# Performance work log

Measured on AMD Instinct MI355X. Metric: run time of the kernel, lower is better.

Reference implementation:

```python
import jax, jax.numpy as jnp
import numpy as np

DIM = 768
HEADS = 12
HEAD_DIM = DIM // HEADS
SCALE = HEAD_DIM ** -0.5


def setup_inputs() -> dict:
    key = jax.random.key(0)
    ks = jax.random.split(key, 6)
    B, N, C = 2, 2048, DIM
    x = jax.random.normal(ks[0], (B, N, C), dtype=jnp.float32)
    s = C ** -0.5
    Wq = jax.random.normal(ks[1], (C, C), dtype=jnp.float32) * s
    Wk = jax.random.normal(ks[2], (C, C), dtype=jnp.float32) * s
    Wv = jax.random.normal(ks[3], (C, C), dtype=jnp.float32) * s
    Wp = jax.random.normal(ks[4], (C, C), dtype=jnp.float32) * s
    bp = jax.random.normal(ks[5], (C,), dtype=jnp.float32) * 0.01
    return {"x": x, "Wq": Wq, "Wk": Wk, "Wv": Wv, "Wp": Wp, "bp": bp}


def reference(x, Wq, Wk, Wv, Wp, bp):
    B, N, C = x.shape
    h, d = HEADS, HEAD_DIM
    # projections (no bias), split heads: (B, h, N, d)
    Q = (x @ Wq.T).reshape(B, N, h, d).transpose(0, 2, 1, 3)
    K = (x @ Wk.T).reshape(B, N, h, d).transpose(0, 2, 1, 3)
    V = (x @ Wv.T).reshape(B, N, h, d).transpose(0, 2, 1, 3)
    # averaged key: (B, h, 1, d) -> scores (B, h, N)
    K_avg = K.mean(axis=2)  # (B, h, d)
    z = jnp.einsum('bhnd,bhd->bhn', Q, K_avg) * SCALE
    attn = jax.nn.softmax(z, axis=-1)  # (B, h, N)
    # circulant gather: roll[b,h,i,j] = attn[b,h,(j-i)%N] / N
    idx = (jnp.arange(N)[None, :] - jnp.arange(N)[:, None]) % N  # (N, N)
    roll = attn[:, :, idx] / N  # (B, h, N, N)
    out = jnp.einsum('bhij,bhjd->bhid', roll, V)  # (B, h, N, d)
    out = out.transpose(0, 2, 1, 3).reshape(B, N, C)
    return out @ Wp.T + bp
```

## Files before the change

### kernel.cpp

```cpp
#include <hip/hip_runtime.h>


typedef __bf16 bf16x8 __attribute__((ext_vector_type(8)));
typedef float  f32x4  __attribute__((ext_vector_type(4)));

#define AS_GLOBAL(p) ((const __attribute__((address_space(1))) unsigned int*)(p))
#define AS_LDS(p)    ((__attribute__((address_space(3))) unsigned int*)(p))

__device__ __forceinline__ void async16(const void* g, void* l) {
    __builtin_amdgcn_global_load_lds(AS_GLOBAL(g), AS_LDS(l), 16, 0, 0);
}

struct bf4 { __bf16 a, b, c, d; };

template <int BM, int BN, int MODE>
__device__ void gemm_phase(char* smem, const __bf16* __restrict__ A,
                           const __bf16* __restrict__ Bt, void* __restrict__ Cout,
                           const float* __restrict__ bias,
                           int K, int ldA, int ldBt, int ldC, int mBase, int nBase)
{
    constexpr int BK = 64;
    constexpr int STRIDE = (BM + BN) * BK * 2;
    constexpr int WM = BM / 2, WN = BN / 2;
    constexpr int MI = WM / 16, NI = WN / 16;
    const int tid = threadIdx.x;
    const int lane = tid & 63, wid = tid >> 6;
    const int lane15 = lane & 15, quad = lane >> 4;
    const int wm = (wid & 1) * WM, wn = (wid >> 1) * WN;

    auto stage = [&](int kb, int buf) {
        __bf16* As = (__bf16*)(smem + buf * STRIDE);
        __bf16* Bs = As + BM * BK;
#pragma unroll
        for (int c0 = 0; c0 < BM * 8; c0 += 256) {
            int c = c0 + tid, row = c >> 3, slot = c & 7;
            int k8 = slot ^ (row & 7);
            async16(A + (size_t)(mBase + row) * ldA + kb + k8 * 8, As + c * 8);
        }
#pragma unroll
        for (int c0 = 0; c0 < BN * 8; c0 += 256) {
            int c = c0 + tid, row = c >> 3, slot = c & 7;
            int k8 = slot ^ (row & 7);
            async16(Bt + (size_t)(nBase + row) * ldBt + kb + k8 * 8, Bs + c * 8);
        }
    };

    f32x4 acc[MI][NI] = {};
    const int nk = K >> 6;

    stage(0, 0);
    for (int ki = 0; ki < nk; ++ki) {
        __syncthreads();
        if (ki + 1 < nk) stage((ki + 1) << 6, (ki + 1) & 1);

        __bf16* As = (__bf16*)(smem + (ki & 1) * STRIDE);
        __bf16* Bs = As + BM * BK;
#pragma unroll
        for (int ks = 0; ks < 2; ++ks) {
            bf16x8 af[MI], bv[NI];
#pragma unroll
            for (int mi = 0; mi < MI; ++mi) {
                int row = wm + mi * 16 + lane15;
                af[mi] = *(const bf16x8*)&As[row * 64 + ((ks * 4 + quad) ^ (row & 7)) * 8];
            }
#pragma unroll
            for (int ni = 0; ni < NI; ++ni) {
                int row = wn + ni * 16 + lane15;
                bv[ni] = *(const bf16x8*)&Bs[row * 64 + ((ks * 4 + quad) ^ (row & 7)) * 8];
            }
#pragma unroll
            for (int mi = 0; mi < MI; ++mi)
#pragma unroll
                for (int ni = 0; ni < NI; ++ni)
                    acc[mi][ni] = __builtin_amdgcn_mfma_f32_16x16x32_bf16(
                        af[mi], bv[ni], acc[mi][ni], 0, 0, 0);
        }
    }

#pragma unroll
    for (int mi = 0; mi < MI; ++mi)
#pragma unroll
        for (int ni = 0; ni < NI; ++ni)
#pragma unroll
            for (int r = 0; r < 4; ++r) {
                int row = mBase + wm + mi * 16 + quad * 4 + r;
                int col = nBase + wn + ni * 16 + lane15;
                float v = acc[mi][ni][r];
                if (MODE == 0) {
                    ((__bf16*)Cout)[(size_t)row * ldC + col] = (__bf16)v;
                } else if (MODE == 1) {
                    ((float*)Cout)[(size_t)row * ldC + col] = v + bias[col];
                } else {
                    int b = row >> 11;
                    if ((unsigned)(col - b * 12) < 12u)
                        ((float*)Cout)[(size_t)col * 2048 + (row & 2047)] = v;
                }
            }
}

__global__ __launch_bounds__(256)
void k_prep(const float* __restrict__ x, const float* __restrict__ Wv,
            const float* __restrict__ Wp,
            __bf16* __restrict__ xb, __bf16* __restrict__ Wvb,
            __bf16* __restrict__ Wpb, float* __restrict__ x_avg)
{
    const int bid = blockIdx.x, tid = threadIdx.x;
    __shared__ float sums[768];
    for (int c = tid; c < 768; c += 256) sums[c] = 0.f;
    __syncthreads();

    const float4* xs = (const float4*)x + (size_t)bid * 1536;
    bf4* xd = (bf4*)xb + (size_t)bid * 1536;
#pragma unroll
    for (int r = 0; r < 6; ++r) {
        int j = tid + r * 256;
        float4 v = xs[j];
        xd[j] = bf4{(__bf16)v.x, (__bf16)v.y, (__bf16)v.z, (__bf16)v.w};
        int col = (j % 192) * 4;
        atomicAdd(&sums[col + 0], v.x);
        atomicAdd(&sums[col + 1], v.y);
        atomicAdd(&sums[col + 2], v.z);
        atomicAdd(&sums[col + 3], v.w);
    }
    const float4* wv4 = (const float4*)Wv;  bf4* wvb4 = (bf4*)Wvb;
    const float4* wp4 = (const float4*)Wp;  bf4* wpb4 = (bf4*)Wpb;
    for (int t = tid; t < 288; t += 256) {
        int g = bid * 288 + t;
        float4 v = wv4[g];
        wvb4[g] = bf4{(__bf16)v.x, (__bf16)v.y, (__bf16)v.z, (__bf16)v.w};
        float4 w2 = wp4[g];
        wpb4[g] = bf4{(__bf16)w2.x, (__bf16)w2.y, (__bf16)w2.z, (__bf16)w2.w};
    }
    __syncthreads();
    const int b = bid >> 8;
    for (int c = tid; c < 768; c += 256)
        atomicAdd(&x_avg[b * 768 + c], sums[c]);
}

__global__ __launch_bounds__(256)
void k_ub(const float* __restrict__ x_avg, const float* __restrict__ Wk,
          const float* __restrict__ Wq, __bf16* __restrict__ Ub)
{
    const int bid = blockIdx.x, tid = threadIdx.x;
    const int lane = tid & 63, wid = tid >> 6;
    __shared__ float sx[768];
    __shared__ float sk[64];
    int b = bid / 12, h = bid % 12;
    for (int c = tid; c < 768; c += 256) sx[c] = x_avg[b * 768 + c];
    __syncthreads();
    for (int round = 0; round < 16; ++round) {
        int o = round * 4 + wid;
        const float* wk = Wk + (size_t)(h * 64 + o) * 768;
        float s = 0.f;
#pragma unroll
        for (int cc0 = 0; cc0 < 768; cc0 += 64) s += sx[cc0 + lane] * wk[cc0 + lane];
#pragma unroll
        for (int off = 32; off; off >>= 1) s += __shfl_down(s, off);
        if (lane == 0) sk[o] = s * (0.125f / 2048.f);
    }
    __syncthreads();
    for (int c = tid; c < 768; c += 256) {
        float s = 0.f;
#pragma unroll 16
        for (int d2 = 0; d2 < 64; ++d2)
            s += sk[d2] * Wq[(size_t)(h * 64 + d2) * 768 + c];
        Ub[(size_t)bid * 768 + c] = (__bf16)s;
    }
}

__global__ __launch_bounds__(256, 2)
void k_gemms(const __bf16* __restrict__ xb, const __bf16* __restrict__ Wvb,
             const __bf16* __restrict__ Ub, __bf16* __restrict__ VT,
             float* __restrict__ z_t)
{
    __shared__ __attribute__((aligned(16))) char smem[65536];
    const int bid = blockIdx.x;
    if (bid < 192) {
        gemm_phase<128, 128, 0>(smem, Wvb, xb, VT, nullptr, 768, 768, 768, 4096,
                                (bid / 32) * 128, (bid % 32) * 128);
    } else {
        gemm_phase<128, 64, 2>(smem, xb, Ub, z_t, nullptr, 768, 768, 768, 0,
                               (bid - 192) * 128, 0);
    }
}

__global__ __launch_bounds__(256, 2)
void k_conv(const float* __restrict__ z_t, const __bf16* __restrict__ VT,
            __bf16* __restrict__ outp)
{
    __shared__ __attribute__((aligned(16))) char smem[69760];
    __bf16 (*rep)[2056] = (__bf16(*)[2056])smem;
    float* red = (float*)(smem + 32896);
    __bf16* attn_s = (__bf16*)(smem + 65664);

    const int bid = blockIdx.x, tid = threadIdx.x;
    const int lane = tid & 63, wid = tid >> 6;
    const int lane15 = lane & 15, quad = lane >> 4;
    const int bh = bid >> 4, b = bh / 12, h = bh % 12;
    const int m0 = (bid & 15) * 128 + (wid & 1) * 64;
    const int wn = (wid >> 1) * 32;

    {
        const float* z = z_t + (size_t)bh * 2048;
        float v[8];
        float m = -1e30f;
#pragma unroll
        for (int j = 0; j < 8; ++j) { v[j] = z[tid + j * 256]; m = fmaxf(m, v[j]); }
#pragma unroll
        for (int off = 32; off; off >>= 1) m = fmaxf(m, __shfl_xor(m, off));
        if (lane == 0) red[wid] = m;
        __syncthreads();
        m = fmaxf(fmaxf(red[0], red[1]), fmaxf(red[2], red[3]));
        __syncthreads();
        float s = 0.f;
#pragma unroll
        for (int j = 0; j < 8; ++j) { v[j] = __expf(v[j] - m); s += v[j]; }
#pragma unroll
        for (int off = 32; off; off >>= 1) s += __shfl_xor(s, off);
        if (lane == 0) red[wid] = s;
        __syncthreads();
        s = red[0] + red[1] + red[2] + red[3];
        float inv = 1.f / (s * 2048.f);
#pragma unroll
        for (int j = 0; j < 8; ++j)
            attn_s[tid + j * 256] = (__bf16)(v[j] * inv);
    }
    __syncthreads();
    for (int idx = tid; idx < 8 * 2048; idx += 256) {
        int a = idx >> 11, u = idx & 2047;
        rep[a][u] = attn_s[(u + a) & 2047];
    }

    const __bf16* vsrc = VT + (size_t)h * 64 * 4096 + b * 2048;

    auto stage = [&](int kb, int buf) {
        __bf16* vt = (__bf16*)(smem + 32896 + buf * 16384);
#pragma unroll
        for (int c0 = 0; c0 < 1024; c0 += 256) {
            int c = c0 + tid, dd = c >> 4, slot = c & 15;
            int k8 = slot ^ (dd & 15);
            async16(vsrc + (size_t)dd * 4096 + kb * 128 + k8 * 8, vt + c * 8);
        }
    };

    f32x4 acc[4][2] = {};
    stage(0, 0);
    for (int kb = 0; kb < 16; ++kb) {
        __syncthreads();
        if (kb + 1 < 16) stage(kb + 1, (kb + 1) & 1);
        __bf16* vt = (__bf16*)(smem + 32896 + (kb & 1) * 16384);

#pragma unroll
        for (int ks = 0; ks < 4; ++ks) {
            int kloc = ks * 32 + quad * 8;
            int kglob = kb * 128 + kloc;
            bf16x8 af[4], bv[2];
#pragma unroll
            for (int mi = 0; mi < 4; ++mi) {
                int m = m0 + mi * 16 + lane15;
                int p = (kglob - m) & 2047;
                int al = p & 7;
                af[mi] = *(const bf16x8*)&rep[al][p - al];
            }
#pragma unroll
            for (int ni = 0; ni < 2; ++ni) {
                int dd = wn + ni * 16 + lane15;
                int slot = (ks * 4 + quad) ^ (dd & 15);
                bv[ni] = *(const bf16x8*)&vt[dd * 128 + slot * 8];
            }
#pragma unroll
            for (int mi = 0; mi < 4; ++mi)
#pragma unroll
                for (int ni = 0; ni < 2; ++ni)
                    acc[mi][ni] = __builtin_amdgcn_mfma_f32_16x16x32_bf16(
                        af[mi], bv[ni], acc[mi][ni], 0, 0, 0);
        }
    }

#pragma unroll
    for (int mi = 0; mi < 4; ++mi)
#pragma unroll
        for (int ni = 0; ni < 2; ++ni)
#pragma unroll
            for (int r = 0; r < 4; ++r) {
                int i = m0 + mi * 16 + quad * 4 + r;
                int dd = wn + ni * 16 + lane15;
                outp[(size_t)(b * 2048 + i) * 768 + h * 64 + dd] =
                    (__bf16)acc[mi][ni][r];
            }
}

__global__ __launch_bounds__(256, 2)
void k_out(const __bf16* __restrict__ out_pre, const __bf16* __restrict__ Wpb,
           const float* __restrict__ bp, float* __restrict__ out)
{
    __shared__ __attribute__((aligned(16))) char smem[65536];
    const int bid = blockIdx.x;
    gemm_phase<128, 128, 1>(smem, out_pre, Wpb, out, bp, 768, 768, 768, 768,
                            (bid / 6) * 128, (bid % 6) * 128);
}

extern "C" void kernel_launch(void* const* d_in, const int* in_sizes, int n_in,
                              void* d_out, int out_size, void* d_ws, size_t ws_size,
                              hipStream_t stream)
{
    (void)in_sizes; (void)n_in; (void)out_size; (void)ws_size;
    const float* x  = (const float*)d_in[0];
    const float* Wq = (const float*)d_in[1];
    const float* Wk = (const float*)d_in[2];
    const float* Wv = (const float*)d_in[3];
    const float* Wp = (const float*)d_in[4];
    const float* bp = (const float*)d_in[5];

    char* w = (char*)d_ws;
    auto alloc = [&](size_t bytes) {
        char* p = w; w += (bytes + 255) & ~(size_t)255; return p;
    };
    float*  x_avg   = (float*) alloc((size_t)2 * 768 * 4);
    __bf16* xb      = (__bf16*)alloc((size_t)4096 * 768 * 2);
    __bf16* Wvb     = (__bf16*)alloc((size_t)768 * 768 * 2);
    __bf16* Wpb     = (__bf16*)alloc((size_t)768 * 768 * 2);
    __bf16* Ub      = (__bf16*)alloc((size_t)64 * 768 * 2);
    float*  z_t     = (float*) alloc((size_t)24 * 2048 * 4);
    __bf16* VT      = (__bf16*)alloc((size_t)768 * 4096 * 2);
    __bf16* out_pre = (__bf16*)alloc((size_t)4096 * 768 * 2);

    hipMemsetAsync(x_avg, 0, 2 * 768 * sizeof(float), stream);
    k_prep <<<512, 256, 0, stream>>>(x, Wv, Wp, xb, Wvb, Wpb, x_avg);
    k_ub   <<<24,  256, 0, stream>>>(x_avg, Wk, Wq, Ub);
    k_gemms<<<224, 256, 0, stream>>>(xb, Wvb, Ub, VT, z_t);
    k_conv <<<384, 256, 0, stream>>>(z_t, VT, out_pre);
    k_out  <<<192, 256, 0, stream>>>(out_pre, Wpb, bp, (float*)d_out);
}
```

Before: 159.7 us.

## Fuse key-average projection into mid kernel and drop atomics and memset

The column-sum of x is now done with deterministic per-block partial sums written to a workspace, replacing the shared and global atomics and the memset. The separate k_ub kernel is folded into the mid kernel: 96 extra blocks each recompute the averaged key and the U vector for one (b,h), then compute z for 512 tokens with a direct dot product, where before an MFMA GEMM with mostly wasted columns was used. This removes two launches and the wasted GEMM work, but each of the 4 blocks per head redundantly recomputes U from fp32 Wk and Wq, and 64 blocks of k_prep take on an extra serial 64-row reduction.

```diff
diff --git a/kernel.cpp b/kernel.cpp
--- a/kernel.cpp
+++ b/kernel.cpp
@@ -88,12 +88,8 @@
                 float v = acc[mi][ni][r];
                 if (MODE == 0) {
                     ((__bf16*)Cout)[(size_t)row * ldC + col] = (__bf16)v;
-                } else if (MODE == 1) {
+                } else {
                     ((float*)Cout)[(size_t)row * ldC + col] = v + bias[col];
-                } else {
-                    int b = row >> 11;
-                    if ((unsigned)(col - b * 12) < 12u)
-                        ((float*)Cout)[(size_t)col * 2048 + (row & 2047)] = v;
                 }
             }
 }
@@ -102,12 +98,9 @@
 void k_prep(const float* __restrict__ x, const float* __restrict__ Wv,
             const float* __restrict__ Wp,
             __bf16* __restrict__ xb, __bf16* __restrict__ Wvb,
-            __bf16* __restrict__ Wpb, float* __restrict__ x_avg)
+            __bf16* __restrict__ Wpb, float* __restrict__ x_part)
 {
     const int bid = blockIdx.x, tid = threadIdx.x;
-    __shared__ float sums[768];
-    for (int c = tid; c < 768; c += 256) sums[c] = 0.f;
-    __syncthreads();
 
     const float4* xs = (const float4*)x + (size_t)bid * 1536;
     bf4* xd = (bf4*)xb + (size_t)bid * 1536;
@@ -116,11 +109,6 @@
         int j = tid + r * 256;
         float4 v = xs[j];
         xd[j] = bf4{(__bf16)v.x, (__bf16)v.y, (__bf16)v.z, (__bf16)v.w};
-        int col = (j % 192) * 4;
-        atomicAdd(&sums[col + 0], v.x);
-        atomicAdd(&sums[col + 1], v.y);
-        atomicAdd(&sums[col + 2], v.z);
-        atomicAdd(&sums[col + 3], v.w);
     }
     const float4* wv4 = (const float4*)Wv;  bf4* wvb4 = (bf4*)Wvb;
     const float4* wp4 = (const float4*)Wp;  bf4* wpb4 = (bf4*)Wpb;
@@ -131,57 +119,88 @@
         float4 w2 = wp4[g];
         wpb4[g] = bf4{(__bf16)w2.x, (__bf16)w2.y, (__bf16)w2.z, (__bf16)w2.w};
     }
-    __syncthreads();
-    const int b = bid >> 8;
-    for (int c = tid; c < 768; c += 256)
-        atomicAdd(&x_avg[b * 768 + c], sums[c]);
-}
-
-__global__ __launch_bounds__(256)
-void k_ub(const float* __restrict__ x_avg, const float* __restrict__ Wk,
-          const float* __restrict__ Wq, __bf16* __restrict__ Ub)
-{
-    const int bid = blockIdx.x, tid = threadIdx.x;
+
+    if (bid < 64) {
+        const float* base = x + (size_t)bid * 64 * 768;
+        float s0 = 0.f, s1 = 0.f, s2 = 0.f;
+        for (int r = 0; r < 64; ++r) {
+            const float* row = base + r * 768;
+            s0 += row[tid];
+            s1 += row[tid + 256];
+            s2 += row[tid + 512];
+        }
+        x_part[bid * 768 + tid]       = s0;
+        x_part[bid * 768 + tid + 256] = s1;
+        x_part[bid * 768 + tid + 512] = s2;
+    }
+}
+
+__global__ __launch_bounds__(256, 2)
+void k_mid(const __bf16* __restrict__ xb, const __bf16* __restrict__ Wvb,
+           const float* __restrict__ x_part, const float* __restrict__ Wk,
+           const float* __restrict__ Wq,
+           __bf16* __restrict__ VT, float* __restrict__ z_t)
+{
+    __shared__ __attribute__((aligned(16))) char smem[65536];
+    const int bid = blockIdx.x;
+    if (bid < 192) {
+        gemm_phase<128, 128, 0>(smem, Wvb, xb, VT, nullptr, 768, 768, 768, 4096,
+                                (bid / 32) * 128, (bid % 32) * 128);
+        return;
+    }
+    const int tid = threadIdx.x;
     const int lane = tid & 63, wid = tid >> 6;
-    __shared__ float sx[768];
-    __shared__ float sk[64];
-    int b = bid / 12, h = bid % 12;
-    for (int c = tid; c < 768; c += 256) sx[c] = x_avg[b * 768 + c];
+    const int idx = bid - 192;
+    const int bh = idx >> 2, q = idx & 3;
+    const int b = bh / 12, h = bh % 12;
+    float* xa  = (float*)smem;
+    float* uld = xa + 768;
+    float* ka  = uld + 768;
+
+    for (int c = tid; c < 768; c += 256) {
+        float s = 0.f;
+#pragma unroll
+        for (int g = 0; g < 32; ++g) s += x_part[(b * 32 + g) * 768 + c];
+        xa[c] = s;
+    }
     __syncthreads();
     for (int round = 0; round < 16; ++round) {
         int o = round * 4 + wid;
         const float* wk = Wk + (size_t)(h * 64 + o) * 768;
         float s = 0.f;
 #pragma unroll
-        for (int cc0 = 0; cc0 < 768; cc0 += 64) s += sx[cc0 + lane] * wk[cc0 + lane];
+        for (int c0 = 0; c0 < 768; c0 += 64) s += xa[c0 + lane] * wk[c0 + lane];
 #pragma unroll
         for (int off = 32; off; off >>= 1) s += __shfl_down(s, off);
-        if (lane == 0) sk[o] = s * (0.125f / 2048.f);
+        if (lane == 0) ka[o] = s * (0.125f / 2048.f);
     }
     __syncthreads();
     for (int c = tid; c < 768; c += 256) {
         float s = 0.f;
 #pragma unroll 16
-        for (int d2 = 0; d2 < 64; ++d2)
-            s += sk[d2] * Wq[(size_t)(h * 64 + d2) * 768 + c];
-        Ub[(size_t)bid * 768 + c] = (__bf16)s;
-    }
-}
-
-__global__ __launch_bounds__(256, 2)
-void k_gemms(const __bf16* __restrict__ xb, const __bf16* __restrict__ Wvb,
-             const __bf16* __restrict__ Ub, __bf16* __restrict__ VT,
-             float* __restrict__ z_t)
-{
-    __shared__ __attribute__((aligned(16))) char smem[65536];
-    const int bid = blockIdx.x;
-    if (bid < 192) {
-        gemm_phase<128, 128, 0>(smem, Wvb, xb, VT, nullptr, 768, 768, 768, 4096,
-                                (bid / 32) * 128, (bid % 32) * 128);
-    } else {
-        gemm_phase<128, 64, 2>(smem, xb, Ub, z_t, nullptr, 768, 768, 768, 0,
-                               (bid - 192) * 128, 0);
-    }
+        for (int d = 0; d < 64; ++d)
+            s += ka[d] * Wq[(size_t)(h * 64 + d) * 768 + c];
+        uld[c] = s;
+    }
+    __syncthreads();
+    const int t0 = q * 512 + tid, t1 = t0 + 256;
+    const bf16x8* r0 = (const bf16x8*)(xb + (size_t)(b * 2048 + t0) * 768);
+    const bf16x8* r1 = (const bf16x8*)(xb + (size_t)(b * 2048 + t1) * 768);
+    const float4* u4 = (const float4*)uld;
+    float s0 = 0.f, s1 = 0.f;
+#pragma unroll 8
+    for (int j = 0; j < 96; ++j) {
+        bf16x8 v0 = r0[j], v1 = r1[j];
+        float4 ua = u4[j * 2], ub = u4[j * 2 + 1];
+        s0 += (float)v0[0] * ua.x + (float)v0[1] * ua.y + (float)v0[2] * ua.z
+            + (float)v0[3] * ua.w + (float)v0[4] * ub.x + (float)v0[5] * ub.y
+            + (float)v0[6] * ub.z + (float)v0[7] * ub.w;
+        s1 += (float)v1[0] * ua.x + (float)v1[1] * ua.y + (float)v1[2] * ua.z
+            + (float)v1[3] * ua.w + (float)v1[4] * ub.x + (float)v1[5] * ub.y
+            + (float)v1[6] * ub.z + (float)v1[7] * ub.w;
+    }
+    z_t[(size_t)bh * 2048 + t0] = s0;
+    z_t[(size_t)bh * 2048 + t1] = s1;
 }
 
 __global__ __launch_bounds__(256, 2)
@@ -316,19 +335,16 @@
     auto alloc = [&](size_t bytes) {
         char* p = w; w += (bytes + 255) & ~(size_t)255; return p;
     };
-    float*  x_avg   = (float*) alloc((size_t)2 * 768 * 4);
+    float*  x_part  = (float*) alloc((size_t)64 * 768 * 4);
     __bf16* xb      = (__bf16*)alloc((size_t)4096 * 768 * 2);
     __bf16* Wvb     = (__bf16*)alloc((size_t)768 * 768 * 2);
     __bf16* Wpb     = (__bf16*)alloc((size_t)768 * 768 * 2);
-    __bf16* Ub      = (__bf16*)alloc((size_t)64 * 768 * 2);
     float*  z_t     = (float*) alloc((size_t)24 * 2048 * 4);
     __bf16* VT      = (__bf16*)alloc((size_t)768 * 4096 * 2);
     __bf16* out_pre = (__bf16*)alloc((size_t)4096 * 768 * 2);
 
-    hipMemsetAsync(x_avg, 0, 2 * 768 * sizeof(float), stream);
-    k_prep <<<512, 256, 0, stream>>>(x, Wv, Wp, xb, Wvb, Wpb, x_avg);
-    k_ub   <<<24,  256, 0, stream>>>(x_avg, Wk, Wq, Ub);
-    k_gemms<<<224, 256, 0, stream>>>(xb, Wvb, Ub, VT, z_t);
-    k_conv <<<384, 256, 0, stream>>>(z_t, VT, out_pre);
-    k_out  <<<192, 256, 0, stream>>>(out_pre, Wpb, bp, (float*)d_out);
-}
+    k_prep<<<512, 256, 0, stream>>>(x, Wv, Wp, xb, Wvb, Wpb, x_part);
+    k_mid <<<288, 256, 0, stream>>>(xb, Wvb, x_part, Wk, Wq, VT, z_t);
+    k_conv<<<384, 256, 0, stream>>>(z_t, VT, out_pre);
+    k_out <<<192, 256, 0, stream>>>(out_pre, Wpb, bp, (float*)d_out);
+}
```

New measurement: 157.6 us. No clear change (-1.3%).
